# Optimization experiments

Measured on AMD Instinct MI355X. Metric: run time of the kernel, lower is better.

## Reference

```python
import jax, jax.numpy as jnp
import numpy as np

D_MODEL = 1024
N_HEADS = 16
LATENT_HEADS = 8
LATENT_DIM = 512
N_LATENTS = 64
WINDOW = 256
HEAD_DIM = D_MODEL // N_HEADS          # 64
LAT_HD = LATENT_DIM // LATENT_HEADS    # 64
B, S = 2, 4096


def setup_inputs() -> dict:
    key = jax.random.key(0)
    ks = jax.random.split(key, 11)
    std = 0.02
    w = lambda k, shp: jax.random.normal(k, shp, jnp.float32) * std
    return {
        'x': jax.random.normal(ks[0], (B, S, D_MODEL), jnp.float32),
        'wq': w(ks[1], (D_MODEL, D_MODEL)),
        'wk': w(ks[2], (D_MODEL, D_MODEL)),
        'wv': w(ks[3], (D_MODEL, D_MODEL)),
        'wgq': w(ks[4], (D_MODEL, LATENT_DIM)),
        'wgk': w(ks[5], (D_MODEL, LATENT_DIM)),
        'wgv': w(ks[6], (D_MODEL, LATENT_DIM)),
        'r_out_w': w(ks[7], (LATENT_DIM, D_MODEL)),
        'gate_local_w': w(ks[8], (N_HEADS, HEAD_DIM)),
        'gate_remote_w': w(ks[9], (N_HEADS, HEAD_DIM)),
        'w_out': w(ks[10], (D_MODEL, D_MODEL)),
    }


def _pool_to_latents(x):
    # x: [B, S, C]; S assumed divisible by N_LATENTS (matches torch path when S % chunk == 0)
    Bx, Sx, C = x.shape
    chunk = max(1, Sx // N_LATENTS)
    return x.reshape(Bx, N_LATENTS, chunk, C).mean(axis=2)  # [B, Nl, C]


def _local_window_attn(Q, K, V):
    # causal sliding-window attention: query i attends keys in [i-WINDOW+1, i]
    Bx, H, Sx, D = Q.shape
    W = WINDOW
    nb = Sx // W
    Qb = Q.reshape(Bx, H, nb, W, D)
    # pad one leading block of keys/values so block b sees key blocks (b-1, b)
    Kp = jnp.pad(K, ((0, 0), (0, 0), (W, 0), (0, 0))).reshape(Bx, H, nb + 1, W, D)
    Vp = jnp.pad(V, ((0, 0), (0, 0), (W, 0), (0, 0))).reshape(Bx, H, nb + 1, W, D)
    Kw = jnp.concatenate([Kp[:, :, :-1], Kp[:, :, 1:]], axis=3)  # [B,H,nb,2W,D]
    Vw = jnp.concatenate([Vp[:, :, :-1], Vp[:, :, 1:]], axis=3)
    i = jnp.arange(W)[:, None]
    j = jnp.arange(2 * W)[None, :]
    # key_pos <= q_pos  <=> j <= i+W ; key_pos >= q_pos-W+1 <=> j > i
    base = (j > i) & (j <= i + W)                       # [W, 2W]
    blk0 = (jnp.arange(nb) > 0)[:, None, None] | (j >= W)[None, :, :]  # pad keys invalid in block 0
    mask = base[None, :, :] & blk0                      # [nb, W, 2W]
    sc = jnp.einsum('bhnid,bhnjd->bhnij', Qb, Kw) / np.sqrt(D).astype(np.float32)
    sc = jnp.where(mask[None, None], sc, -jnp.inf)
    p = jax.nn.softmax(sc, axis=-1)
    out = jnp.einsum('bhnij,bhnjd->bhnid', p, Vw)
    return out.reshape(Bx, H, Sx, D)


def reference(x, wq, wk, wv, wgq, wgk, wgv, r_out_w, gate_local_w, gate_remote_w, w_out):
    Bx, Sx, _ = x.shape
    chunk = max(1, Sx // N_LATENTS)
    # local path projections: [B, H, S, Dh]
    Q = (x @ wq).reshape(Bx, Sx, N_HEADS, HEAD_DIM).transpose(0, 2, 1, 3)
    K = (x @ wk).reshape(Bx, Sx, N_HEADS, HEAD_DIM).transpose(0, 2, 1, 3)
    V = (x @ wv).reshape(Bx, Sx, N_HEADS, HEAD_DIM).transpose(0, 2, 1, 3)
    local = _local_window_attn(Q, K, V)                 # [B, H, S, Dh]
    # latent (remote) path: GQ over mean-pooled latents, chunk-causal
    GQ = (x @ wgq).reshape(Bx, Sx, LATENT_HEADS, LAT_HD).transpose(0, 2, 1, 3)   # [B,Lh,S,Ld]
    GK = _pool_to_latents(x @ wgk).reshape(Bx, N_LATENTS, LATENT_HEADS, LAT_HD).transpose(0, 2, 1, 3)
    GV = _pool_to_latents(x @ wgv).reshape(Bx, N_LATENTS, LATENT_HEADS, LAT_HD).transpose(0, 2, 1, 3)
    lsc = jnp.einsum('bhsd,bhnd->bhsn', GQ, GK) / np.sqrt(LAT_HD).astype(np.float32)
    lmask = jnp.arange(N_LATENTS)[None, :] <= (jnp.arange(Sx) // chunk)[:, None]  # [S, Nl]
    lsc = jnp.where(lmask[None, None], lsc, -jnp.inf)
    lp = jax.nn.softmax(lsc, axis=-1)
    rem = jnp.einsum('bhsn,bhnd->bhsd', lp, GV)          # [B, Lh, S, Ld]
    rem = rem.transpose(0, 2, 1, 3).reshape(Bx, Sx, LATENT_DIM) @ r_out_w  # [B, S, d_model]
    rem = rem.reshape(Bx, Sx, N_HEADS, HEAD_DIM).transpose(0, 2, 1, 3)     # [B, H, S, Dh]
    # learned per-head gates computed from the query
    gl = jax.nn.sigmoid(jnp.einsum('bhsd,hd->bhs', Q, gate_local_w))[..., None]
    gr = jax.nn.sigmoid(jnp.einsum('bhsd,hd->bhs', Q, gate_remote_w))[..., None]
    out = gl * local + gr * rem                          # [B, H, S, Dh]
    out = out.transpose(0, 2, 1, 3).reshape(Bx, Sx, D_MODEL)
    return out @ w_out
```

## Files before the change

### kernel.cpp

```cpp
#include <hip/hip_runtime.h>

#define AS1 __attribute__((address_space(1)))
#define AS3 __attribute__((address_space(3)))

typedef float    f32x4  __attribute__((ext_vector_type(4)));
typedef __bf16   bf16x8 __attribute__((ext_vector_type(8)));
typedef __bf16   bf16x4 __attribute__((ext_vector_type(4)));
typedef unsigned int u32x4 __attribute__((ext_vector_type(4)));

static constexpr int SEQ = 4096, NBATCH = 2, DMODEL = 1024, NHEADS = 16, HDIM = 64;
static constexpr int LHEADS = 8, LDIM = 512, NLAT = 64, WIN = 256;
static constexpr int BSROWS = NBATCH * SEQ;
static constexpr int QKVN = 3584;
static constexpr int KOFF = 1024, VOFF = 2048, GQOFF = 3072;

struct TJ { const float* in; __bf16* out; int K; int N; };
struct TJ8 { TJ j[8]; };
__global__ __launch_bounds__(256) void prep_all(const float* __restrict__ x,
                                                __bf16* __restrict__ xb,
                                                __bf16* __restrict__ xpool, TJ8 jobs) {
    __shared__ float tbuf[32][33];
    int bid = blockIdx.x, t = threadIdx.x;
    if (bid < 512) {
        int bn = bid >> 2;
        int c  = (bid & 3) * 256 + t;
        const float* p = x + (size_t)bn * 64 * 1024 + c;
        __bf16* q = xb + (size_t)bn * 64 * 1024 + c;
        float s = 0.f;
        #pragma unroll 8
        for (int j = 0; j < 64; ++j) {
            float v = p[(size_t)j * 1024];
            q[(size_t)j * 1024] = (__bf16)v;
            s += v;
        }
        xpool[(size_t)bn * 1024 + c] = (__bf16)(s * 0.015625f);
    } else {
        int ti = bid - 512;
        TJ jb = jobs.j[ti >> 10];
        int rem = ti & 1023;
        int k0 = (rem >> 5) * 32, n0 = (rem & 31) * 32;
        if (k0 >= jb.K || n0 >= jb.N) return;
        int tx = t & 31, ty = t >> 5;
        #pragma unroll
        for (int i = ty; i < 32; i += 8) tbuf[i][tx] = jb.in[(size_t)(k0 + i) * jb.N + n0 + tx];
        __syncthreads();
        #pragma unroll
        for (int i = ty; i < 32; i += 8) jb.out[(size_t)(n0 + i) * jb.K + k0 + tx] = (__bf16)tbuf[tx][i];
    }
}

template <bool EPI, bool OUTBF>
__global__ __launch_bounds__(256) void gemm_bf16(const __bf16* __restrict__ A,
                                                 const __bf16* __restrict__ Bt,
                                                 int M, int N, int K,
                                                 __bf16* __restrict__ outb,
                                                 float* __restrict__ outf,
                                                 const __bf16* __restrict__ lcl,
                                                 const float* __restrict__ grb) {
    __shared__ alignas(16) __bf16 sA[128 * 64];
    __shared__ alignas(16) __bf16 sB[128 * 64];
    int t = threadIdx.x, w = t >> 6, l = t & 63;
    int m0 = blockIdx.x * 128, n0 = blockIdx.y * 128;
    int wr = w >> 1, wc = w & 1;
    int lr = l & 15, lk = (l >> 4) * 8;

    f32x4 zero = {0.f, 0.f, 0.f, 0.f};
    f32x4 acc[4][4];
    #pragma unroll
    for (int a = 0; a < 4; ++a)
        #pragma unroll
        for (int b2 = 0; b2 < 4; ++b2) acc[a][b2] = zero;

    for (int kt = 0; kt < K; kt += 64) {
        #pragma unroll
        for (int c = 0; c < 4; ++c) {
            int lin  = w * 64 + c * 256;
            int linl = lin + l;
            int row = linl >> 3, c8 = (linl & 7) * 8;
            __builtin_amdgcn_global_load_lds(
                (const AS1 void*)(A + (size_t)(m0 + row) * K + kt + c8),
                (AS3 void*)((char*)sA + (size_t)lin * 16), 16, 0, 0);
            __builtin_amdgcn_global_load_lds(
                (const AS1 void*)(Bt + (size_t)(n0 + row) * K + kt + c8),
                (AS3 void*)((char*)sB + (size_t)lin * 16), 16, 0, 0);
        }
        __syncthreads();
        #pragma unroll
        for (int ks = 0; ks < 2; ++ks) {
            bf16x8 av[4], bv[4];
            #pragma unroll
            for (int mi = 0; mi < 4; ++mi)
                av[mi] = *(const bf16x8*)(sA + (wr * 64 + mi * 16 + lr) * 64 + ks * 32 + lk);
            #pragma unroll
            for (int ni = 0; ni < 4; ++ni)
                bv[ni] = *(const bf16x8*)(sB + (wc * 64 + ni * 16 + lr) * 64 + ks * 32 + lk);
            #pragma unroll
            for (int mi = 0; mi < 4; ++mi)
                #pragma unroll
                for (int ni = 0; ni < 4; ++ni)
                    acc[mi][ni] = __builtin_amdgcn_mfma_f32_16x16x32_bf16(
                        av[mi], bv[ni], acc[mi][ni], 0, 0, 0);
        }
        __syncthreads();
    }

    int cr = (l >> 4) * 4, cc = l & 15;
    #pragma unroll
    for (int mi = 0; mi < 4; ++mi) {
        #pragma unroll
        for (int ni = 0; ni < 4; ++ni) {
            int col = n0 + wc * 64 + ni * 16 + cc;
            #pragma unroll
            for (int r = 0; r < 4; ++r) {
                int row = m0 + wr * 64 + mi * 16 + cr + r;
                float v = acc[mi][ni][r];
                if constexpr (EPI) {
                    v = (float)lcl[(size_t)row * 1024 + col] +
                        grb[(size_t)row * 16 + (col >> 6)] * v;
                }
                if constexpr (OUTBF) outb[(size_t)row * N + col] = (__bf16)v;
                else                 outf[(size_t)row * N + col] = v;
            }
        }
    }
}

#define BAR() do { __builtin_amdgcn_sched_barrier(0); __builtin_amdgcn_s_barrier(); \
                   __builtin_amdgcn_sched_barrier(0); } while (0)
#define LGK0() do { asm volatile("s_waitcnt lgkmcnt(0)" ::: "memory"); \
                    __builtin_amdgcn_sched_barrier(0); } while (0)
#define VMC(n) do { asm volatile("s_waitcnt vmcnt(" #n ")" ::: "memory"); \
                    __builtin_amdgcn_sched_barrier(0); } while (0)
#define STG(gp, regionbase, rowbase, ktc) do { \
    int row_ = (rowbase) + (t >> 3); \
    int tc_ = (t & 7) ^ ((t >> 3) & 7); \
    __builtin_amdgcn_global_load_lds( \
        (const AS1 void*)((gp) + (size_t)row_ * K + (ktc) + tc_ * 8), \
        (AS3 void*)(lds + (regionbase) + (rowbase) * 128 + w * 1024), 16, 0, 0); \
} while (0)
#define LOADA(buf, qm) do { \
    _Pragma("unroll") for (int ai_ = 0; ai_ < 4; ++ai_) \
    _Pragma("unroll") for (int ks_ = 0; ks_ < 2; ++ks_) \
        a[ai_][ks_] = *(const bf16x8*)(lds + ((((buf) * 65536) + \
            (wm * 128 + (qm) * 64 + ai_ * 16 + l15) * 128 + ks_ * 64 + l4 * 16) ^ rswz)); \
} while (0)
#define LOADB2(buf, half) do { \
    _Pragma("unroll") for (int j_ = 0; j_ < 2; ++j_) \
    _Pragma("unroll") for (int ks_ = 0; ks_ < 2; ++ks_) \
        b2[j_][ks_] = *(const bf16x8*)(lds + ((((buf) * 65536 + 32768) + \
            (wn * 64 + ((half) * 2 + j_) * 16 + l15) * 128 + ks_ * 64 + l4 * 16) ^ rswz)); \
} while (0)
#define MFMA_PH(qm, half) do { \
    __builtin_amdgcn_s_setprio(1); \
    _Pragma("unroll") for (int ai_ = 0; ai_ < 4; ++ai_) \
    _Pragma("unroll") for (int j_ = 0; j_ < 2; ++j_) { \
        f32x4 c_ = acc[(qm) * 4 + ai_][(half) * 2 + j_]; \
        c_ = __builtin_amdgcn_mfma_f32_16x16x32_bf16(a[ai_][0], b2[j_][0], c_, 0, 0, 0); \
        c_ = __builtin_amdgcn_mfma_f32_16x16x32_bf16(a[ai_][1], b2[j_][1], c_, 0, 0, 0); \
        acc[(qm) * 4 + ai_][(half) * 2 + j_] = c_; \
    } \
    __builtin_amdgcn_s_setprio(0); \
} while (0)

__global__ __launch_bounds__(512, 2) void gemm256_bf16(
    const __bf16* __restrict__ A, const __bf16* __restrict__ Bt,
    int M, int N, int K, __bf16* __restrict__ outb, __bf16* __restrict__ Vt) {
    __shared__ char lds[131072];
    const int t = threadIdx.x, w = t >> 6, l = t & 63;
    const int wm = w >> 2, wn = w & 3;
    const int l15 = l & 15, l4 = l >> 4;
    const int m0 = blockIdx.x * 256, n0 = blockIdx.y * 256;
    const int NT = K >> 6;
    const int rswz = (l15 & 7) << 4;

    f32x4 acc[8][4];
    #pragma unroll
    for (int i = 0; i < 8; ++i)
        #pragma unroll
        for (int j = 0; j < 4; ++j) acc[i][j] = (f32x4){0.f, 0.f, 0.f, 0.f};
    bf16x8 a[4][2], b2[2][2];

    const __bf16* Ab = A + (size_t)m0 * K;
    const __bf16* Bb = Bt + (size_t)n0 * K;

    STG(Ab, 0, 0, 0);        STG(Ab, 0, 128, 0);
    STG(Ab, 0, 64, 0);       STG(Ab, 0, 192, 0);
    STG(Bb, 32768, 0, 0);    STG(Bb, 32768, 64, 0);
    STG(Bb, 32768, 128, 0);  STG(Bb, 32768, 192, 0);
    STG(Ab, 65536, 0, 64);   STG(Ab, 65536, 128, 64);
    VMC(2); BAR();

    int it = 0;
    for (; it + 3 < NT; it += 2) {
        const int kt1 = (it + 1) << 6, kt2 = (it + 2) << 6, kt3 = (it + 3) << 6;
        LOADA(0, 0); LOADB2(0, 0);
        STG(Ab, 65536, 64, kt1); STG(Ab, 65536, 192, kt1);
        BAR(); LGK0(); MFMA_PH(0, 0); BAR();
        LOADB2(0, 1);
        STG(Bb, 98304, 0, kt1); STG(Bb, 98304, 64, kt1);
        BAR(); LGK0(); MFMA_PH(0, 1); BAR();
        LOADA(0, 1); LOADB2(0, 0);
        STG(Bb, 98304, 128, kt1); STG(Bb, 98304, 192, kt1);
        BAR(); LGK0(); MFMA_PH(1, 0); BAR();
        LOADB2(0, 1);
        STG(Ab, 0, 0, kt2); STG(Ab, 0, 128, kt2);
        BAR(); LGK0(); MFMA_PH(1, 1); VMC(2); BAR();
        LOADA(1, 0); LOADB2(1, 0);
        STG(Ab, 0, 64, kt2); STG(Ab, 0, 192, kt2);
        BAR(); LGK0(); MFMA_PH(0, 0); BAR();
        LOADB2(1, 1);
        STG(Bb, 32768, 0, kt2); STG(Bb, 32768, 64, kt2);
        BAR(); LGK0(); MFMA_PH(0, 1); BAR();
        LOADA(1, 1); LOADB2(1, 0);
        STG(Bb, 32768, 128, kt2); STG(Bb, 32768, 192, kt2);
        BAR(); LGK0(); MFMA_PH(1, 0); BAR();
        LOADB2(1, 1);
        STG(Ab, 65536, 0, kt3); STG(Ab, 65536, 128, kt3);
        BAR(); LGK0(); MFMA_PH(1, 1); VMC(2); BAR();
    }
    {
        const int kt1 = (it + 1) << 6;
        LOADA(0, 0); LOADB2(0, 0);
        STG(Ab, 65536, 64, kt1); STG(Ab, 65536, 192, kt1);
        BAR(); LGK0(); MFMA_PH(0, 0); BAR();
        LOADB2(0, 1);
        STG(Bb, 98304, 0, kt1); STG(Bb, 98304, 64, kt1);
        BAR(); LGK0(); MFMA_PH(0, 1); BAR();
        LOADA(0, 1); LOADB2(0, 0);
        STG(Bb, 98304, 128, kt1); STG(Bb, 98304, 192, kt1);
        BAR(); LGK0(); MFMA_PH(1, 0); BAR();
        LOADB2(0, 1);
        BAR(); LGK0(); MFMA_PH(1, 1); VMC(0); BAR();
        LOADA(1, 0); LOADB2(1, 0);
        BAR(); LGK0(); MFMA_PH(0, 0); BAR();
        LOADB2(1, 1);
        BAR(); LGK0(); MFMA_PH(0, 1); BAR();
        LOADA(1, 1); LOADB2(1, 0);
        BAR(); LGK0(); MFMA_PH(1, 0); BAR();
        LOADB2(1, 1);
        LGK0(); MFMA_PH(1, 1);
    }

    int cr = l4 * 4, cc = l15;
    if (Vt != nullptr && n0 >= VOFF && n0 < GQOFF) {
        #pragma unroll
        for (int mi = 0; mi < 8; ++mi) {
            #pragma unroll
            for (int ni = 0; ni < 4; ++ni) {
                int vcol = (n0 - VOFF) + wn * 64 + ni * 16 + cc;
                int row0 = m0 + wm * 128 + mi * 16 + cr;
                int bb = row0 >> 12, ss = row0 & 4095;
                bf16x4 pk;
                #pragma unroll
                for (int r = 0; r < 4; ++r) pk[r] = (__bf16)acc[mi][ni][r];
                *(bf16x4*)(Vt + ((size_t)bb * DMODEL + vcol) * SEQ + ss) = pk;
            }
        }
    } else {
        #pragma unroll
        for (int mi = 0; mi < 8; ++mi) {
            #pragma unroll
            for (int ni = 0; ni < 4; ++ni) {
                int col = n0 + wn * 64 + ni * 16 + cc;
                #pragma unroll
                for (int r = 0; r < 4; ++r) {
                    int row = m0 + wm * 128 + mi * 16 + cr + r;
                    outb[(size_t)row * N + col] = (__bf16)acc[mi][ni][r];
                }
            }
        }
    }
}
#undef BAR
#undef LGK0
#undef VMC
#undef STG
#undef LOADA
#undef LOADB2
#undef MFMA_PH

__global__ __launch_bounds__(256, 2) void attn_fused(
    const __bf16* __restrict__ QKVG, const __bf16* __restrict__ Vt,
    const __bf16* __restrict__ GKV,
    const float* __restrict__ glw, const float* __restrict__ grw,
    __bf16* __restrict__ outl, float* __restrict__ grbuf,
    __bf16* __restrict__ rem) {
    __shared__ alignas(16) char smem[81920];
    int t = threadIdx.x, w = t >> 6, l = t & 63;
    int l15 = l & 15, l4 = l >> 4;
    int b = blockIdx.z;
    f32x4 zero = {0.f, 0.f, 0.f, 0.f};

    if (blockIdx.y < 16) {
        int blk = blockIdx.x, h = blockIdx.y;
        char* sKb = smem;
        char* sPb = smem + 65536;

        bf16x8 qf[4][2];
        long qbase = (long)b * SEQ + blk * 256 + 64 * w;
        #pragma unroll
        for (int qq = 0; qq < 4; ++qq)
            #pragma unroll
            for (int ks = 0; ks < 2; ++ks)
                qf[qq][ks] = *(const bf16x8*)(QKVG + (size_t)(qbase + qq * 16 + l15) * QKVN
                                              + h * 64 + ks * 32 + l4 * 8);

        long g0 = (long)b * SEQ + (long)(blk - 1) * WIN;
        #pragma unroll
        for (int rep = 0; rep < 16; ++rep) {
            int ci = rep * 256 + t;
            int row = ci >> 3, c8 = (ci & 7) * 8;
            u32x4 kv = {0u, 0u, 0u, 0u};
            if (!(blk == 0 && row < 256))
                kv = *(const u32x4*)(QKVG + (size_t)(g0 + row) * QKVN + KOFF + h * 64 + c8);
            *(u32x4*)(sKb + row * 128 + ((c8 * 2) ^ ((row & 7) << 4))) = kv;
        }

        float dlp[4], drp[4];
        #pragma unroll
        for (int qq = 0; qq < 4; ++qq) {
            float dl = 0.f, dr = 0.f;
            #pragma unroll
            for (int ks = 0; ks < 2; ++ks) {
                const float* gp = glw + h * 64 + ks * 32 + l4 * 8;
                const float* rp = grw + h * 64 + ks * 32 + l4 * 8;
                #pragma unroll
                for (int j = 0; j < 8; ++j) {
                    float qv = (float)qf[qq][ks][j];
                    dl += qv * gp[j];
                    dr += qv * rp[j];
                }
            }
            dlp[qq] = dl; drp[qq] = dr;
        }
        float glv[4], grv[4];
        #pragma unroll
        for (int qq = 0; qq < 4; ++qq) {
            float dl = dlp[qq] + __shfl_xor(dlp[qq], 16);
            dl += __shfl_xor(dl, 32);
            float dr = drp[qq] + __shfl_xor(drp[qq], 16);
            dr += __shfl_xor(dr, 32);
            glv[qq] = 1.f / (1.f + __expf(-dl));
            grv[qq] = 1.f / (1.f + __expf(-dr));
        }
        if (l4 == 0) {
            #pragma unroll
            for (int qq = 0; qq < 4; ++qq)
                grbuf[(size_t)(qbase + qq * 16 + l15) * 16 + h] = grv[qq];
        }
        __syncthreads();

        f32x4 acc[4][4];
        #pragma unroll
        for (int a2 = 0; a2 < 4; ++a2)
            #pragma unroll
            for (int d = 0; d < 4; ++d) acc[a2][d] = zero;
        float psum[4] = {0.f, 0.f, 0.f, 0.f};

        char* sPw = sPb + w * 4096;
        int nsteps = (w == 3) ? 10 : 11;
        int kk0 = 64 * w;
        const __bf16* vtb = Vt + (size_t)b * DMODEL * SEQ + (size_t)(h * 64) * SEQ;

        for (int stp = 0; stp < nsteps; ++stp) {
            int kk = kk0 + 32 * stp;
            f32x4 sacc[2][4];
            #pragma unroll
            for (int kt2 = 0; kt2 < 2; ++kt2) {
                int krow = kk + kt2 * 16 + l15;
                int swz = (krow & 7) << 4;
                bf16x8 af0 = *(const bf16x8*)(sKb + krow * 128 + ((l4 * 16) ^ swz));
                bf16x8 af1 = *(const bf16x8*)(sKb + krow * 128 + ((64 + l4 * 16) ^ swz));
                #pragma unroll
                for (int qq = 0; qq < 4; ++qq) {
                    f32x4 s = __builtin_amdgcn_mfma_f32_16x16x32_bf16(af0, qf[qq][0], zero, 0, 0, 0);
                    sacc[kt2][qq] = __builtin_amdgcn_mfma_f32_16x16x32_bf16(af1, qf[qq][1], s, 0, 0, 0);
                }
            }
            #pragma unroll
            for (int qq = 0; qq < 4; ++qq) {
                int qloc = 64 * w + qq * 16 + l15;
                int prow = qq * 16 + l15;
                #pragma unroll
                for (int kt2 = 0; kt2 < 2; ++kt2) {
                    int jb = kk + kt2 * 16 + l4 * 4;
                    bf16x4 pb;
                    #pragma unroll
                    for (int r = 0; r < 4; ++r) {
                        int jw = jb + r;
                        bool act = (jw > qloc) && (jw <= qloc + 256) && (blk > 0 || jw >= 256);
                        float pv = act ? __expf(sacc[kt2][qq][r] * 0.125f) : 0.f;
                        psum[qq] += pv;
                        pb[r] = (__bf16)pv;
                    }
                    *(bf16x4*)(sPw + prow * 64 + ((kt2 * 32 + l4 * 8) ^ ((prow & 3) << 4))) = pb;
                }
            }
            int kglob = (blk - 1) * WIN + kk + l4 * 8;
            if (kglob < 0) kglob = 0;
            bf16x8 pa[4], bv[4];
            #pragma unroll
            for (int qq = 0; qq < 4; ++qq) {
                int prow = qq * 16 + l15;
                pa[qq] = *(const bf16x8*)(sPw + prow * 64 + ((l4 * 16) ^ ((prow & 3) << 4)));
            }
            #pragma unroll
            for (int dt = 0; dt < 4; ++dt)
                bv[dt] = *(const bf16x8*)(vtb + (size_t)(dt * 16 + l15) * SEQ + kglob);
            #pragma unroll
            for (int qq = 0; qq < 4; ++qq)
                #pragma unroll
                for (int dt = 0; dt < 4; ++dt)
                    acc[qq][dt] = __builtin_amdgcn_mfma_f32_16x16x32_bf16(pa[qq], bv[dt], acc[qq][dt], 0, 0, 0);
        }

        float cmb[4];
        #pragma unroll
        for (int qq = 0; qq < 4; ++qq) {
            float s = psum[qq] + __shfl_xor(psum[qq], 16);
            s += __shfl_xor(s, 32);
            cmb[qq] = glv[qq] / s;
        }
        #pragma unroll
        for (int qq = 0; qq < 4; ++qq) {
            #pragma unroll
            for (int r = 0; r < 4; ++r) {
                float sc = __shfl(cmb[qq], l4 * 4 + r, 64);
                size_t row = (size_t)(qbase + qq * 16 + l4 * 4 + r);
                __bf16* op = outl + row * DMODEL + h * 64 + l15;
                #pragma unroll
                for (int dt = 0; dt < 4; ++dt)
                    op[dt * 16] = (__bf16)(acc[qq][dt][r] * sc);
            }
        }
    } else {
        int sb = blockIdx.x, lh = blockIdx.y - 16;
        char* sK  = smem;
        char* sVt = smem + 8192;
        char* sPb = smem + 16384;

        bf16x8 qf[4][2];
        long qbase = (long)b * SEQ + sb * 256 + 64 * w;
        #pragma unroll
        for (int qq = 0; qq < 4; ++qq)
            #pragma unroll
            for (int ks = 0; ks < 2; ++ks)
                qf[qq][ks] = *(const bf16x8*)(QKVG + (size_t)(qbase + qq * 16 + l15) * QKVN
                                              + GQOFF + lh * 64 + ks * 32 + l4 * 8);

        #pragma unroll
        for (int rep = 0; rep < 2; ++rep) {
            int ci = rep * 256 + t;
            int row = ci >> 3, c8 = (ci & 7) * 8;
            u32x4 kv = *(const u32x4*)(GKV + (size_t)(b * 64 + row) * 1024 + lh * 64 + c8);
            *(u32x4*)(sK + row * 128 + ((c8 * 2) ^ ((row & 7) << 4))) = kv;
        }
        #pragma unroll
        for (int rep = 0; rep < 16; ++rep) {
            int idx = rep * 256 + t;
            int d = idx & 63, n = idx >> 6;
            __bf16 v = GKV[(size_t)(b * 64 + n) * 1024 + 512 + lh * 64 + d];
            *(__bf16*)(sVt + d * 128 + ((n * 2) ^ ((d & 7) << 4))) = v;
        }
        __syncthreads();

        f32x4 acc[4][4];
        #pragma unroll
        for (int a2 = 0; a2 < 4; ++a2)
            #pragma unroll
            for (int d = 0; d < 4; ++d) acc[a2][d] = zero;
        float psum[4] = {0.f, 0.f, 0.f, 0.f};

        char* sPw = sPb + w * 4096;
        int qloc0 = sb * 256 + 64 * w;

        #pragma unroll
        for (int stp = 0; stp < 2; ++stp) {
            int kk = 32 * stp;
            f32x4 sacc[2][4];
            #pragma unroll
            for (int kt2 = 0; kt2 < 2; ++kt2) {
                int krow = kk + kt2 * 16 + l15;
                int swz = (krow & 7) << 4;
                bf16x8 af0 = *(const bf16x8*)(sK + krow * 128 + ((l4 * 16) ^ swz));
                bf16x8 af1 = *(const bf16x8*)(sK + krow * 128 + ((64 + l4 * 16) ^ swz));
                #pragma unroll
                for (int qq = 0; qq < 4; ++qq) {
                    f32x4 s = __builtin_amdgcn_mfma_f32_16x16x32_bf16(af0, qf[qq][0], zero, 0, 0, 0);
                    sacc[kt2][qq] = __builtin_amdgcn_mfma_f32_16x16x32_bf16(af1, qf[qq][1], s, 0, 0, 0);
                }
            }
            #pragma unroll
            for (int qq = 0; qq < 4; ++qq) {
                int qdv = (qloc0 + qq * 16 + l15) >> 6;
                int prow = qq * 16 + l15;
                #pragma unroll
                for (int kt2 = 0; kt2 < 2; ++kt2) {
                    int nb = kk + kt2 * 16 + l4 * 4;
                    bf16x4 pb;
                    #pragma unroll
                    for (int r = 0; r < 4; ++r) {
                        int n = nb + r;
                        float pv = (n <= qdv) ? __expf(sacc[kt2][qq][r] * 0.125f) : 0.f;
                        psum[qq] += pv;
                        pb[r] = (__bf16)pv;
                    }
                    *(bf16x4*)(sPw + prow * 64 + ((kt2 * 32 + l4 * 8) ^ ((prow & 3) << 4))) = pb;
                }
            }
            bf16x8 pa[4], bv[4];
            #pragma unroll
            for (int qq = 0; qq < 4; ++qq) {
                int prow = qq * 16 + l15;
                pa[qq] = *(const bf16x8*)(sPw + prow * 64 + ((l4 * 16) ^ ((prow & 3) << 4)));
            }
            #pragma unroll
            for (int dt = 0; dt < 4; ++dt) {
                int d = dt * 16 + l15;
                bv[dt] = *(const bf16x8*)(sVt + d * 128 + ((kk * 2 + l4 * 16) ^ ((d & 7) << 4)));
            }
            #pragma unroll
            for (int qq = 0; qq < 4; ++qq)
                #pragma unroll
                for (int dt = 0; dt < 4; ++dt)
                    acc[qq][dt] = __builtin_amdgcn_mfma_f32_16x16x32_bf16(pa[qq], bv[dt], acc[qq][dt], 0, 0, 0);
        }

        float cmb[4];
        #pragma unroll
        for (int qq = 0; qq < 4; ++qq) {
            float s = psum[qq] + __shfl_xor(psum[qq], 16);
            s += __shfl_xor(s, 32);
            cmb[qq] = 1.f / s;
        }
        #pragma unroll
        for (int qq = 0; qq < 4; ++qq) {
            #pragma unroll
            for (int r = 0; r < 4; ++r) {
                float sc = __shfl(cmb[qq], l4 * 4 + r, 64);
                size_t row = (size_t)(qbase + qq * 16 + l4 * 4 + r);
                __bf16* op = rem + row * LDIM + lh * 64 + l15;
                #pragma unroll
                for (int dt = 0; dt < 4; ++dt)
                    op[dt * 16] = (__bf16)(acc[qq][dt][r] * sc);
            }
        }
    }
}

extern "C" void kernel_launch(void* const* d_in, const int* in_sizes, int n_in,
                              void* d_out, int out_size, void* d_ws, size_t ws_size,
                              hipStream_t stream) {
    (void)in_sizes; (void)n_in; (void)out_size; (void)ws_size;
    const float* x    = (const float*)d_in[0];
    const float* wq   = (const float*)d_in[1];
    const float* wk   = (const float*)d_in[2];
    const float* wv   = (const float*)d_in[3];
    const float* wgq  = (const float*)d_in[4];
    const float* wgk  = (const float*)d_in[5];
    const float* wgv  = (const float*)d_in[6];
    const float* rout = (const float*)d_in[7];
    const float* glw  = (const float*)d_in[8];
    const float* grw  = (const float*)d_in[9];
    const float* wout = (const float*)d_in[10];

    char* p = (char*)d_ws;
    auto alloc = [&](size_t bytes) {
        char* r = p;
        p += (bytes + 255) & ~(size_t)255;
        return r;
    };
    __bf16* xb    = (__bf16*)alloc((size_t)BSROWS * DMODEL * 2);
    __bf16* QKVG  = (__bf16*)alloc((size_t)BSROWS * QKVN * 2);
    __bf16* VtG   = (__bf16*)alloc((size_t)BSROWS * DMODEL * 2);
    __bf16* wcatT = (__bf16*)alloc((size_t)QKVN * DMODEL * 2);
    __bf16* woutT = (__bf16*)alloc((size_t)DMODEL * DMODEL * 2);
    __bf16* wgkvT = (__bf16*)alloc((size_t)1024 * DMODEL * 2);
    __bf16* routT = (__bf16*)alloc((size_t)DMODEL * LDIM * 2);
    __bf16* xpool = (__bf16*)alloc((size_t)128 * DMODEL * 2);
    __bf16* GKVb  = (__bf16*)alloc((size_t)128 * 1024 * 2);
    __bf16* localg= (__bf16*)alloc((size_t)BSROWS * DMODEL * 2);
    float*  grbuf = (float*) alloc((size_t)BSROWS * 16 * 4);
    __bf16* remb  = (__bf16*)alloc((size_t)BSROWS * LDIM * 2);
    __bf16* outpre = xb;

    TJ8 jobs;
    jobs.j[0] = {wq,   wcatT,                 DMODEL, DMODEL};
    jobs.j[1] = {wk,   wcatT + 1024 * DMODEL, DMODEL, DMODEL};
    jobs.j[2] = {wv,   wcatT + 2048 * DMODEL, DMODEL, DMODEL};
    jobs.j[3] = {wgq,  wcatT + 3072 * DMODEL, DMODEL, LDIM};
    jobs.j[4] = {wout, woutT,                 DMODEL, DMODEL};
    jobs.j[5] = {wgk,  wgkvT,                 DMODEL, LDIM};
    jobs.j[6] = {wgv,  wgkvT + 512 * DMODEL,  DMODEL, LDIM};
    jobs.j[7] = {rout, routT,                 LDIM,   DMODEL};

    prep_all<<<dim3(512 + 8192), 256, 0, stream>>>(x, xb, xpool, jobs);

    gemm256_bf16<<<dim3(32, 14), 512, 0, stream>>>(xb, wcatT, BSROWS, QKVN, DMODEL, QKVG, VtG);
    gemm_bf16<false, true><<<dim3(1, 8), 256, 0, stream>>>(xpool, wgkvT, 128, 1024, DMODEL, GKVb, nullptr, nullptr, nullptr);

    attn_fused<<<dim3(16, 24, 2), 256, 0, stream>>>(QKVG, VtG, GKVb, glw, grw,
                                                    localg, grbuf, remb);

    gemm_bf16<true, true><<<dim3(64, 8), 256, 0, stream>>>(remb, routT, BSROWS, DMODEL, LDIM, outpre, nullptr, localg, grbuf);
    gemm_bf16<false, false><<<dim3(64, 8), 256, 0, stream>>>(outpre, woutT, BSROWS, DMODEL, DMODEL, nullptr, (float*)d_out, nullptr, nullptr);
}
```

Measured before the change: 203.6 us.

## Fold latent KV GEMM into QKV GEMM grid and read K directly from global

The small pooled-latent GK/GV projection is moved into extra blocks of the big 256x256 QKV GEMM launch, with xpool padded to 256 rows and zero-filled by prep_all so the tile shape fits. This removes a separate kernel launch and its serialization. Separately, the local attention kernel stops staging the 512-row K window into 64KB of LDS and instead loads K fragments straight from global memory. That cuts shared memory use and may raise occupancy, but K rows are re-read from global/L2 by each wave.

```diff
diff --git a/kernel.cpp b/kernel.cpp
--- a/kernel.cpp
+++ b/kernel.cpp
@@ -34,7 +34,7 @@
             s += v;
         }
         xpool[(size_t)bn * 1024 + c] = (__bf16)(s * 0.015625f);
-    } else {
+    } else if (bid < 8704) {
         int ti = bid - 512;
         TJ jb = jobs.j[ti >> 10];
         int rem = ti & 1023;
@@ -46,6 +46,12 @@
         __syncthreads();
         #pragma unroll
         for (int i = ty; i < 32; i += 8) jb.out[(size_t)(n0 + i) * jb.K + k0 + tx] = (__bf16)tbuf[tx][i];
+    } else {
+        int zi = bid - 8704;
+        size_t idx = ((size_t)zi * 256 + t) * 16;
+        u32x4 z = {0u, 0u, 0u, 0u};
+        *(u32x4*)(xpool + 128 * 1024 + idx)     = z;
+        *(u32x4*)(xpool + 128 * 1024 + idx + 8) = z;
     }
 }
 
@@ -164,14 +170,27 @@
 
 __global__ __launch_bounds__(512, 2) void gemm256_bf16(
     const __bf16* __restrict__ A, const __bf16* __restrict__ Bt,
-    int M, int N, int K, __bf16* __restrict__ outb, __bf16* __restrict__ Vt) {
+    int M, int N, int K, __bf16* __restrict__ outb, __bf16* __restrict__ Vt,
+    const __bf16* __restrict__ A2, const __bf16* __restrict__ B2,
+    __bf16* __restrict__ out2) {
     __shared__ char lds[131072];
     const int t = threadIdx.x, w = t >> 6, l = t & 63;
     const int wm = w >> 2, wn = w & 3;
     const int l15 = l & 15, l4 = l >> 4;
-    const int m0 = blockIdx.x * 256, n0 = blockIdx.y * 256;
     const int NT = K >> 6;
     const int rswz = (l15 & 7) << 4;
+
+    const __bf16* Ab; const __bf16* Bb; __bf16* outp; int Nout, m0, n0; bool doVt;
+    if (blockIdx.y == 14) {
+        if (blockIdx.x >= 4) return;
+        m0 = 0; n0 = blockIdx.x * 256;
+        Ab = A2; Bb = B2 + (size_t)n0 * K;
+        outp = out2; Nout = 1024; doVt = false;
+    } else {
+        m0 = blockIdx.x * 256; n0 = blockIdx.y * 256;
+        Ab = A + (size_t)m0 * K; Bb = Bt + (size_t)n0 * K;
+        outp = outb; Nout = N; doVt = (n0 >= VOFF && n0 < GQOFF);
+    }
 
     f32x4 acc[8][4];
     #pragma unroll
@@ -179,9 +198,6 @@
         #pragma unroll
         for (int j = 0; j < 4; ++j) acc[i][j] = (f32x4){0.f, 0.f, 0.f, 0.f};
     bf16x8 a[4][2], b2[2][2];
-
-    const __bf16* Ab = A + (size_t)m0 * K;
-    const __bf16* Bb = Bt + (size_t)n0 * K;
 
     STG(Ab, 0, 0, 0);        STG(Ab, 0, 128, 0);
     STG(Ab, 0, 64, 0);       STG(Ab, 0, 192, 0);
@@ -242,7 +258,7 @@
     }
 
     int cr = l4 * 4, cc = l15;
-    if (Vt != nullptr && n0 >= VOFF && n0 < GQOFF) {
+    if (doVt) {
         #pragma unroll
         for (int mi = 0; mi < 8; ++mi) {
             #pragma unroll
@@ -265,7 +281,7 @@
                 #pragma unroll
                 for (int r = 0; r < 4; ++r) {
                     int row = m0 + wm * 128 + mi * 16 + cr + r;
-                    outb[(size_t)row * N + col] = (__bf16)acc[mi][ni][r];
+                    outp[(size_t)row * Nout + col] = (__bf16)acc[mi][ni][r];
                 }
             }
         }
@@ -285,7 +301,7 @@
     const float* __restrict__ glw, const float* __restrict__ grw,
     __bf16* __restrict__ outl, float* __restrict__ grbuf,
     __bf16* __restrict__ rem) {
-    __shared__ alignas(16) char smem[81920];
+    __shared__ alignas(16) char smem[32768];
     int t = threadIdx.x, w = t >> 6, l = t & 63;
     int l15 = l & 15, l4 = l >> 4;
     int b = blockIdx.z;
@@ -293,8 +309,7 @@
 
     if (blockIdx.y < 16) {
         int blk = blockIdx.x, h = blockIdx.y;
-        char* sKb = smem;
-        char* sPb = smem + 65536;
+        char* sPb = smem;
 
         bf16x8 qf[4][2];
         long qbase = (long)b * SEQ + blk * 256 + 64 * w;
@@ -304,17 +319,6 @@
             for (int ks = 0; ks < 2; ++ks)
                 qf[qq][ks] = *(const bf16x8*)(QKVG + (size_t)(qbase + qq * 16 + l15) * QKVN
                                               + h * 64 + ks * 32 + l4 * 8);
-
-        long g0 = (long)b * SEQ + (long)(blk - 1) * WIN;
-        #pragma unroll
-        for (int rep = 0; rep < 16; ++rep) {
-            int ci = rep * 256 + t;
-            int row = ci >> 3, c8 = (ci & 7) * 8;
-            u32x4 kv = {0u, 0u, 0u, 0u};
-            if (!(blk == 0 && row < 256))
-                kv = *(const u32x4*)(QKVG + (size_t)(g0 + row) * QKVN + KOFF + h * 64 + c8);
-            *(u32x4*)(sKb + row * 128 + ((c8 * 2) ^ ((row & 7) << 4))) = kv;
-        }
 
         float dlp[4], drp[4];
         #pragma unroll
@@ -348,7 +352,6 @@
             for (int qq = 0; qq < 4; ++qq)
                 grbuf[(size_t)(qbase + qq * 16 + l15) * 16 + h] = grv[qq];
         }
-        __syncthreads();
 
         f32x4 acc[4][4];
         #pragma unroll
@@ -360,6 +363,7 @@
         char* sPw = sPb + w * 4096;
         int nsteps = (w == 3) ? 10 : 11;
         int kk0 = 64 * w;
+        long g0 = (long)b * SEQ + (long)(blk - 1) * WIN;
         const __bf16* vtb = Vt + (size_t)b * DMODEL * SEQ + (size_t)(h * 64) * SEQ;
 
         for (int stp = 0; stp < nsteps; ++stp) {
@@ -368,9 +372,11 @@
             #pragma unroll
             for (int kt2 = 0; kt2 < 2; ++kt2) {
                 int krow = kk + kt2 * 16 + l15;
-                int swz = (krow & 7) << 4;
-                bf16x8 af0 = *(const bf16x8*)(sKb + krow * 128 + ((l4 * 16) ^ swz));
-                bf16x8 af1 = *(const bf16x8*)(sKb + krow * 128 + ((64 + l4 * 16) ^ swz));
+                long kgrow = g0 + krow;
+                if (blk == 0 && krow < 256) kgrow = (long)b * SEQ;
+                const __bf16* kp = QKVG + (size_t)kgrow * QKVN + KOFF + h * 64;
+                bf16x8 af0 = *(const bf16x8*)(kp + l4 * 8);
+                bf16x8 af1 = *(const bf16x8*)(kp + 32 + l4 * 8);
                 #pragma unroll
                 for (int qq = 0; qq < 4; ++qq) {
                     f32x4 s = __builtin_amdgcn_mfma_f32_16x16x32_bf16(af0, qf[qq][0], zero, 0, 0, 0);
@@ -577,8 +583,8 @@
     __bf16* woutT = (__bf16*)alloc((size_t)DMODEL * DMODEL * 2);
     __bf16* wgkvT = (__bf16*)alloc((size_t)1024 * DMODEL * 2);
     __bf16* routT = (__bf16*)alloc((size_t)DMODEL * LDIM * 2);
-    __bf16* xpool = (__bf16*)alloc((size_t)128 * DMODEL * 2);
-    __bf16* GKVb  = (__bf16*)alloc((size_t)128 * 1024 * 2);
+    __bf16* xpool = (__bf16*)alloc((size_t)256 * DMODEL * 2);
+    __bf16* GKVb  = (__bf16*)alloc((size_t)256 * 1024 * 2);
     __bf16* localg= (__bf16*)alloc((size_t)BSROWS * DMODEL * 2);
     float*  grbuf = (float*) alloc((size_t)BSROWS * 16 * 4);
     __bf16* remb  = (__bf16*)alloc((size_t)BSROWS * LDIM * 2);
@@ -594,10 +600,10 @@
     jobs.j[6] = {wgv,  wgkvT + 512 * DMODEL,  DMODEL, LDIM};
     jobs.j[7] = {rout, routT,                 LDIM,   DMODEL};
 
-    prep_all<<<dim3(512 + 8192), 256, 0, stream>>>(x, xb, xpool, jobs);
-
-    gemm256_bf16<<<dim3(32, 14), 512, 0, stream>>>(xb, wcatT, BSROWS, QKVN, DMODEL, QKVG, VtG);
-    gemm_bf16<false, true><<<dim3(1, 8), 256, 0, stream>>>(xpool, wgkvT, 128, 1024, DMODEL, GKVb, nullptr, nullptr, nullptr);
+    prep_all<<<dim3(512 + 8192 + 32), 256, 0, stream>>>(x, xb, xpool, jobs);
+
+    gemm256_bf16<<<dim3(32, 15), 512, 0, stream>>>(xb, wcatT, BSROWS, QKVN, DMODEL,
+                                                   QKVG, VtG, xpool, wgkvT, GKVb);
 
     attn_fused<<<dim3(16, 24, 2), 256, 0, stream>>>(QKVG, VtG, GKVb, glw, grw,
                                                     localg, grbuf, remb);
```

Result: faster. 176.3 us (-13.4%).
